# Optimization experiments

Hardware: AMD Instinct MI355X
Metric: run time of the kernel (lower is better)

Reference implementation:

```python
import jax, jax.numpy as jnp
import numpy as np

INPUT_SIZE = 32   # activity vocab
HIDDEN = 512
OUT = 33          # OUT-1 activity logits + 1 duration
COND = 128
LAYERS = 2
MAXLEN = 64
BATCH = 256
SOS = 0
SLOPE = 0.01      # LeakyReLU default negative slope

def _leaky(x):
    return jnp.where(x >= 0, x, SLOPE * x)

def setup_inputs() -> dict:
    key = jax.random.key(0)
    ks = jax.random.split(key, 16)
    s = 0.05  # small init scale keeps gates in a sane range
    return {
        "batch_size": BATCH,
        "h0": jax.random.normal(ks[0], (LAYERS, BATCH, HIDDEN), jnp.float32),
        "c0": jax.random.normal(ks[1], (LAYERS, BATCH, HIDDEN), jnp.float32),
        "conditionals": jax.random.normal(ks[2], (BATCH, COND), jnp.float32),
        "emb": jax.random.normal(ks[3], (INPUT_SIZE, HIDDEN - 1), jnp.float32) * s,
        "Wih": jax.random.normal(ks[4], (LAYERS, 4 * HIDDEN, HIDDEN), jnp.float32) * s,
        "Whh": jax.random.normal(ks[5], (LAYERS, 4 * HIDDEN, HIDDEN), jnp.float32) * s,
        "bih": jax.random.normal(ks[6], (LAYERS, 4 * HIDDEN), jnp.float32) * s,
        "bhh": jax.random.normal(ks[7], (LAYERS, 4 * HIDDEN), jnp.float32) * s,
        "fcW": jax.random.normal(ks[8], (HIDDEN, COND), jnp.float32) * s,
        "fcb": jax.random.normal(ks[9], (HIDDEN,), jnp.float32) * s,
        "fc2W": jax.random.normal(ks[10], (HIDDEN, HIDDEN), jnp.float32) * s,
        "fc2b": jax.random.normal(ks[11], (HIDDEN,), jnp.float32) * s,
        "fc3W": jax.random.normal(ks[12], (OUT, HIDDEN), jnp.float32) * s,
        "fc3b": jax.random.normal(ks[13], (OUT,), jnp.float32) * s,
    }

def reference(batch_size, h0, c0, conditionals, emb, Wih, Whh, bih, bhh,
              fcW, fcb, fc2W, fc2b, fc3W, fc3b):
    B = h0.shape[1]
    # conditionals branch is step-invariant: compute once (same math as per-step fc+LeakyReLU)
    cond = _leaky(conditionals @ fcW.T + fcb)  # [B, H]
    # decoder_input = zeros[B,1,2] with act channel = sos
    inp0 = jnp.concatenate(
        [jnp.full((B, 1), float(SOS), jnp.float32), jnp.zeros((B, 1), jnp.float32)], axis=-1)

    def step(carry, _):
        h, c, inp = carry  # h,c: [L,B,H], inp: [B,2]
        # CustomDurationEmbedding: embed act index, concat duration channel -> [B,H]
        x = jnp.concatenate([emb[inp[:, 0].astype(jnp.int32)], inp[:, 1:]], axis=-1)
        hs, cs = [], []
        for l in range(LAYERS):  # seq_len==1 per step -> one LSTM cell per layer
            g = x @ Wih[l].T + bih[l] + h[l] @ Whh[l].T + bhh[l]  # [B,4H]
            i_g, f_g, g_g, o_g = jnp.split(g, 4, axis=-1)         # torch gate order i,f,g,o
            c_l = jax.nn.sigmoid(f_g) * c[l] + jax.nn.sigmoid(i_g) * jnp.tanh(g_g)
            h_l = jax.nn.sigmoid(o_g) * jnp.tanh(c_l)
            hs.append(h_l); cs.append(c_l)
            x = h_l
        h_new, c_new = jnp.stack(hs), jnp.stack(cs)
        # conditional_add: (lstm_out + cond) -> fc2 -> LeakyReLU -> fc3
        pred = _leaky((x + cond) @ fc2W.T + fc2b) @ fc3W.T + fc3b  # [B,OUT]
        # pack: topk(1) over activity logits; softmax over singleton seq dim == 1.0
        act = jnp.argmax(pred[:, :OUT - 1], axis=-1).astype(pred.dtype)[:, None]
        dur = jnp.ones((B, 1), pred.dtype)
        nxt = jnp.concatenate([act, dur], axis=-1)
        return (h_new, c_new, nxt), pred

    _, outs = jax.lax.scan(step, (h0, c0, inp0), None, length=MAXLEN)  # [T,B,OUT]
    outs = jnp.transpose(outs, (1, 0, 2))  # [B,T,OUT]
    acts_log_probs = jax.nn.log_softmax(outs[..., :OUT - 1], axis=-1)
    durations = jax.nn.softmax(outs[..., OUT - 1:], axis=1)  # Softmax(dim=-2): over time
    return jnp.concatenate([acts_log_probs, durations], axis=-1)
```

## Files before the change

### kernel.cpp

```cpp
#include <hip/hip_runtime.h>
#include <math.h>

#define BB   256
#define HH   512
#define NWG  256
#define NTHR 1024
#define TT   64
#define NOUT 33
#define CD   128
#define SZ   (HH*BB)
#define LOFF (4*HH*HH)
#define BOFF (4*HH)
#define WBLK (16*1024)

typedef float f16v __attribute__((ext_vector_type(16)));
typedef float f8v  __attribute__((ext_vector_type(8)));
typedef const __attribute__((address_space(4))) float  cfloat;
typedef const __attribute__((address_space(4))) f16v   cf16v;
typedef const __attribute__((address_space(4))) f8v    cf8v;

__device__ __forceinline__ float sigm(float x)  { return 1.0f/(1.0f+expf(-x)); }
__device__ __forceinline__ float lrelu(float x) { return x >= 0.0f ? x : 0.01f*x; }

__device__ __forceinline__ float gld(const float* p) {
  return __hip_atomic_load(p, __ATOMIC_RELAXED, __HIP_MEMORY_SCOPE_AGENT);
}
__device__ __forceinline__ void gst(float* p, float v) {
  __hip_atomic_store(p, v, __ATOMIC_RELAXED, __HIP_MEMORY_SCOPE_AGENT);
}

__device__ __forceinline__ cfloat* cptr(const float* p) {
  unsigned long long u = (unsigned long long)p;
  unsigned lo = __builtin_amdgcn_readfirstlane((unsigned)u);
  unsigned hi = __builtin_amdgcn_readfirstlane((unsigned)(u >> 32));
  return (cfloat*)((((unsigned long long)hi) << 32) | (unsigned long long)lo);
}

__device__ __forceinline__ void gbar(unsigned* bar, unsigned ep, int grp, bool fence) {
  __syncthreads();
  if (threadIdx.x == 0) {
    if (fence) __builtin_amdgcn_fence(__ATOMIC_RELEASE, "agent");
    unsigned old = __hip_atomic_fetch_add(&bar[grp*16], 1u, __ATOMIC_RELAXED, __HIP_MEMORY_SCOPE_AGENT);
    if (old == ep*32u + 31u) {
      unsigned o2 = __hip_atomic_fetch_add(&bar[128], 1u, __ATOMIC_RELAXED, __HIP_MEMORY_SCOPE_AGENT);
      if (o2 == ep*8u + 7u)
        __hip_atomic_store(&bar[144], ep+1u, __ATOMIC_RELAXED, __HIP_MEMORY_SCOPE_AGENT);
    }
    while (__hip_atomic_load(&bar[144], __ATOMIC_RELAXED, __HIP_MEMORY_SCOPE_AGENT) < ep+1u)
      __builtin_amdgcn_s_sleep(1);
    if (fence) __builtin_amdgcn_fence(__ATOMIC_ACQUIRE, "agent");
  }
  __syncthreads();
}

extern "C" __global__ void __launch_bounds__(256)
transpose_weights(const float* __restrict__ Wih, const float* __restrict__ Whh,
                  float* __restrict__ wsT)
{
  const int w   = blockIdx.x;
  const int tid = threadIdx.x;
  float* dst = wsT + w*WBLK;
  #pragma unroll 1
  for (int j = 0; j < 64; ++j) {
    int i  = j*256 + tid;
    int ri = i >> 10, k = i & 1023;
    int l  = k >> 9,  kk = k & 511;
    int r2 = ri & 7,  u = r2 >> 2, g = r2 & 3;
    const float* src = (ri < 8) ? Wih : Whh;
    dst[k*16 + ri] = src[l*LOFF + (g*HH + 2*w + u)*HH + kk];
  }
}

__device__ __forceinline__ void FMA2(const f16v& w, float x0, float x1,
                                     float h0, float h1, float* acc) {
  #pragma unroll
  for (int r = 0; r < 8; ++r) {
    acc[r*2+0] += w[r]*x0;
    acc[r*2+1] += w[r]*x1;
  }
  #pragma unroll
  for (int r = 0; r < 8; ++r) {
    acc[r*2+0] += w[8+r]*h0;
    acc[r*2+1] += w[8+r]*h1;
  }
}

__device__ __forceinline__ void lstm_phase(const float* __restrict__ wT,
    const float* __restrict__ bias, float* __restrict__ red,
    const float* __restrict__ xsrc, const float* __restrict__ hsrc,
    float* __restrict__ hdst, float* __restrict__ cbuf,
    int hu0, int tid, int ks, int bg)
{
  const int lane  = tid & 63;
  const int kbase = ks*64;
  const int b0    = bg*128 + lane;
  cf16v* wk = (cf16v*)cptr(wT + kbase*16);
  const float* xp = xsrc + kbase*BB + b0;
  const float* hp = hsrc + kbase*BB + b0;

  float acc[16];
  #pragma unroll
  for (int r = 0; r < 16; ++r) acc[r] = 0.0f;

  float qx[4], qh[4], px[4], ph[4];
  #pragma unroll
  for (int j = 0; j < 2; ++j) {
    qx[j*2] = gld(xp + j*BB); qx[j*2+1] = gld(xp + j*BB + 64);
    qh[j*2] = gld(hp + j*BB); qh[j*2+1] = gld(hp + j*BB + 64);
  }
  #pragma unroll 1
  for (int it = 0; it < 32; ++it) {
    f16v w0 = wk[it*2+0];
    f16v w1 = wk[it*2+1];
    if (it+1 < 32) {
      #pragma unroll
      for (int j = 0; j < 2; ++j) {
        px[j*2]   = gld(xp + (it*2+2+j)*BB);  px[j*2+1] = gld(xp + (it*2+2+j)*BB + 64);
        ph[j*2]   = gld(hp + (it*2+2+j)*BB);  ph[j*2+1] = gld(hp + (it*2+2+j)*BB + 64);
      }
    }
    FMA2(w0, qx[0], qx[1], qh[0], qh[1], acc);
    FMA2(w1, qx[2], qx[3], qh[2], qh[3], acc);
    #pragma unroll
    for (int j = 0; j < 4; ++j) { qx[j] = px[j]; qh[j] = ph[j]; }
  }
  #pragma unroll
  for (int r = 0; r < 8; ++r) {
    red[(ks*8 + r)*BB + b0]      = acc[r*2];
    red[(ks*8 + r)*BB + b0 + 64] = acc[r*2+1];
  }
  __syncthreads();
  if (tid < 512) {
    const int b = tid & 255, u = tid >> 8;
    float g[4];
    #pragma unroll
    for (int gg = 0; gg < 4; ++gg) {
      float s = bias[u*4+gg];
      #pragma unroll
      for (int k2 = 0; k2 < 8; ++k2) s += red[(k2*8 + u*4+gg)*BB + b];
      g[gg] = s;
    }
    const int hu = hu0 + u;
    float ig = sigm(g[0]), fg = sigm(g[1]);
    float gv = tanhf(g[2]), og = sigm(g[3]);
    float cn = fg*cbuf[hu*BB+b] + ig*gv;
    cbuf[hu*BB+b] = cn;
    gst(hdst + hu*BB + b, og*tanhf(cn));
  }
}

extern "C" __global__ void __launch_bounds__(NTHR)
decoder_kernel(const float* __restrict__ h0, const float* __restrict__ c0,
               const float* __restrict__ conds, const float* __restrict__ emb,
               const float* __restrict__ wsT, const float* __restrict__ bih,
               const float* __restrict__ bhh, const float* __restrict__ fcW,
               const float* __restrict__ fcb, const float* __restrict__ fc2W,
               const float* __restrict__ fc2b, const float* __restrict__ fc3W,
               const float* __restrict__ fc3b,
               float* __restrict__ out, unsigned* bar, float* wsf)
{
  const int w   = blockIdx.x;
  const int tid = threadIdx.x;
  const int hu0 = 2*w;
  const int grp = w & 7;
  const int wv  = tid >> 6;
  const int bg  = wv & 1;
  const int ks  = wv >> 1;

  float* xbuf  = wsf;
  float* h1b0  = wsf + 1*SZ;
  float* h1b1  = wsf + 2*SZ;
  float* h2b0  = wsf + 3*SZ;
  float* h2b1  = wsf + 4*SZ;
  float* c1b   = wsf + 5*SZ;
  float* c2b   = wsf + 6*SZ;
  float* condb = wsf + 7*SZ;
  float* yb    = wsf + 8*SZ;
  float* condY = wsf + 9*SZ;

  const float* wT1 = wsT + w*WBLK;
  const float* wT2 = wsT + w*WBLK + 512*16;

  __shared__ float red[64*BB];
  __shared__ float bias1[8], bias2[8], biasc[2];
  __shared__ float lds_y[HH];
  __shared__ float part[NOUT][17];
  __shared__ int   lds_act;
  __shared__ float lds_pad[4096];
  if (tid == 0) ((volatile float*)lds_pad)[0] = 0.0f;

  if (tid < 512) {
    const int b = tid & 255, u = tid >> 8;
    const int k = hu0 + u;
    xbuf[k*BB+b] = (k < HH-1) ? emb[k] : 0.0f;
    h1b0[k*BB+b] = h0[b*HH + k];
    c1b [k*BB+b] = c0[b*HH + k];
    h2b0[k*BB+b] = h0[(BB+b)*HH + k];
    c2b [k*BB+b] = c0[(BB+b)*HH + k];
    float a = fcb[k];
    const float4* cp = (const float4*)(conds + b*CD);
    const float4* wp = (const float4*)(fcW + k*CD);
    #pragma unroll 8
    for (int q = 0; q < CD/4; ++q) {
      float4 c4 = cp[q], w4 = wp[q];
      a += c4.x*w4.x + c4.y*w4.y + c4.z*w4.z + c4.w*w4.w;
    }
    condb[k*BB+b] = lrelu(a);
  }
  if (tid < 8) {
    int u = tid >> 2, g = tid & 3;
    bias1[tid] = bih[g*HH + hu0 + u] + bhh[g*HH + hu0 + u];
    bias2[tid] = bih[BOFF + g*HH + hu0 + u] + bhh[BOFF + g*HH + hu0 + u];
  }
  if (tid < 2) biasc[tid] = fc2b[hu0 + tid];

  unsigned ep = 0;
  gbar(bar, ep++, grp, true);

  if (tid < 512) {
    const int b = tid & 255, u = tid >> 8;
    cfloat* wr = cptr(fc2W + (hu0+u)*HH);
    float s = 0.0f;
    #pragma unroll 4
    for (int k = 0; k < HH; k += 4) {
      s += wr[k]*condb[k*BB+b]     + wr[k+1]*condb[(k+1)*BB+b]
         + wr[k+2]*condb[(k+2)*BB+b] + wr[k+3]*condb[(k+3)*BB+b];
    }
    condY[(hu0+u)*BB + b] = s;
  }
  __syncthreads();

  for (int t = 0; t < TT; ++t) {
    const bool par = (t & 1) != 0;
    float* h1r = par ? h1b1 : h1b0;
    float* h1w = par ? h1b0 : h1b1;
    float* h2r = par ? h2b1 : h2b0;
    float* h2w = par ? h2b0 : h2b1;

    lstm_phase(wT1, bias1, red, xbuf, h1r, h1w, c1b, hu0, tid, ks, bg);
    gbar(bar, ep++, grp, false);
    lstm_phase(wT2, bias2, red, h1w, h2r, h2w, c2b, hu0, tid, ks, bg);
    gbar(bar, ep++, grp, false);
    {
      const int b = tid & 255, s4 = tid >> 8;
      const float* hp = h2w + (s4*128)*BB + b;
      cf8v* w0v = (cf8v*)cptr(fc2W + (hu0+0)*HH + s4*128);
      cf8v* w1v = (cf8v*)cptr(fc2W + (hu0+1)*HH + s4*128);
      float a0 = 0.0f, a1 = 0.0f;
      float q[8], pq[8];
      #pragma unroll
      for (int j = 0; j < 8; ++j) q[j] = gld(hp + j*BB);
      #pragma unroll 1
      for (int it = 0; it < 16; ++it) {
        f8v wa = w0v[it];
        f8v wb = w1v[it];
        if (it+1 < 16) {
          #pragma unroll
          for (int j = 0; j < 8; ++j) pq[j] = gld(hp + (it*8+8+j)*BB);
        }
        #pragma unroll
        for (int j = 0; j < 8; ++j) { a0 += wa[j]*q[j]; a1 += wb[j]*q[j]; }
        #pragma unroll
        for (int j = 0; j < 8; ++j) q[j] = pq[j];
      }
      red[(s4*2+0)*BB + b] = a0;
      red[(s4*2+1)*BB + b] = a1;
    }
    __syncthreads();
    if (tid < 512) {
      const int b = tid & 255, u = tid >> 8;
      float s = biasc[u] + condY[(hu0+u)*BB + b];
      #pragma unroll
      for (int s4 = 0; s4 < 4; ++s4) s += red[(s4*2+u)*BB + b];
      gst(yb + (hu0+u)*BB + b, lrelu(s));
    }
    gbar(bar, ep++, grp, false);
    {
      if (tid < 512) lds_y[tid] = gld(yb + tid*BB + w);
      __syncthreads();
      int o = 0, kc = 0;
      bool active = false;
      if (tid < 512)        { o = tid & 31; kc = tid >> 5; active = true; }
      else if (tid < 528)   { o = 32;       kc = tid - 512; active = true; }
      if (active) {
        float p = 0.0f;
        const float* fw = fc3W + o*HH + kc*32;
        #pragma unroll
        for (int k2 = 0; k2 < 32; ++k2) p += fw[k2] * lds_y[kc*32 + k2];
        part[o][kc] = p;
      }
      __syncthreads();
      float predv = -1e30f;
      if (tid < NOUT) {
        float s = fc3b[tid];
        #pragma unroll
        for (int kc2 = 0; kc2 < 16; ++kc2) s += part[tid][kc2];
        predv = s;
        out[(w*TT + t)*NOUT + tid] = s;
      }
      if (tid < 64) {
        float v  = (tid < 32) ? predv : -1e30f;
        int  idx = tid;
        #pragma unroll
        for (int off = 32; off > 0; off >>= 1) {
          float ov = __shfl_xor(v, off);
          int   oi = __shfl_xor(idx, off);
          if (ov > v || (ov == v && oi < idx)) { v = ov; idx = oi; }
        }
        if (tid == 0) lds_act = idx;
      }
      __syncthreads();
      const int act = lds_act;
      if (tid < 512)
        gst(xbuf + tid*BB + w, (tid < 511) ? emb[act*(HH-1) + tid] : 1.0f);
    }
    gbar(bar, ep++, grp, false);
  }

  if (tid < TT) {
    const int s = tid;
    float* po = out + (w*TT + s)*NOUT;
    float v[NOUT];
    #pragma unroll
    for (int o = 0; o < NOUT; ++o) v[o] = po[o];
    float m = v[0];
    #pragma unroll
    for (int o = 1; o < 32; ++o) m = fmaxf(m, v[o]);
    float sum = 0.0f;
    #pragma unroll
    for (int o = 0; o < 32; ++o) sum += expf(v[o] - m);
    float lse = m + logf(sum);
    #pragma unroll
    for (int o = 0; o < 32; ++o) po[o] = v[o] - lse;
    float d = v[32];
    float dm = d;
    #pragma unroll
    for (int off = 32; off > 0; off >>= 1) dm = fmaxf(dm, __shfl_xor(dm, off));
    float e = expf(d - dm);
    float es = e;
    #pragma unroll
    for (int off = 32; off > 0; off >>= 1) es += __shfl_xor(es, off);
    po[32] = e / es;
  }
}

extern "C" void kernel_launch(void* const* d_in, const int* in_sizes, int n_in,
                              void* d_out, int out_size, void* d_ws, size_t ws_size,
                              hipStream_t stream) {
  const float* h0   = (const float*)d_in[1];
  const float* c0   = (const float*)d_in[2];
  const float* cnd  = (const float*)d_in[3];
  const float* emb  = (const float*)d_in[4];
  const float* Wih  = (const float*)d_in[5];
  const float* Whh  = (const float*)d_in[6];
  const float* bih  = (const float*)d_in[7];
  const float* bhh  = (const float*)d_in[8];
  const float* fcW  = (const float*)d_in[9];
  const float* fcb  = (const float*)d_in[10];
  const float* fc2W = (const float*)d_in[11];
  const float* fc2b = (const float*)d_in[12];
  const float* fc3W = (const float*)d_in[13];
  const float* fc3b = (const float*)d_in[14];

  unsigned* bar = (unsigned*)d_ws;
  float* wsf = (float*)((char*)d_ws + 1024);
  float* wsT = wsf + 10*SZ;

  (void)hipMemsetAsync(d_ws, 0, 1024, stream);

  hipLaunchKernelGGL(transpose_weights, dim3(NWG), dim3(256), 0, stream,
                     Wih, Whh, wsT);
  hipLaunchKernelGGL(decoder_kernel, dim3(NWG), dim3(NTHR), 0, stream,
                     h0, c0, cnd, emb, wsT, bih, bhh, fcW, fcb,
                     fc2W, fc2b, fc3W, fc3b, (float*)d_out, bar, wsf);
}
```

Before: 3.731 ms.

## Retile LSTM decoder into 64 hidden-slices by 4 batch-groups with per-group barriers

Repartitions the persistent decoder so each of 256 workgroups owns 8 hidden units across a 64-batch tile instead of 2 hidden units across all 256 batches. Activations move to a k-interleaved float4 layout and are staged through double-buffered LDS while pre-transposed weights are read as scalar-uniform vectors. The grid barrier now synchronizes only the 64 workgroups sharing a batch group, and the cell state lives in registers. fc2 weights are also pre-transposed. This cuts grid-wide sync cost and global traffic per step, but it adds more LDS staging and syncthreads per phase.

```diff
diff --git a/kernel.cpp b/kernel.cpp
--- a/kernel.cpp
+++ b/kernel.cpp
@@ -3,21 +3,20 @@
 
 #define BB   256
 #define HH   512
-#define NWG  256
-#define NTHR 1024
 #define TT   64
 #define NOUT 33
 #define CD   128
-#define SZ   (HH*BB)
+#define NTHR 1024
 #define LOFF (4*HH*HH)
-#define BOFF (4*HH)
-#define WBLK (16*1024)
+
+#define HUT  8
+#define BT   64
+#define ABUF 131072
+#define FC2OFF 4194304
 
 typedef float f16v __attribute__((ext_vector_type(16)));
-typedef float f8v  __attribute__((ext_vector_type(8)));
-typedef const __attribute__((address_space(4))) float  cfloat;
-typedef const __attribute__((address_space(4))) f16v   cf16v;
-typedef const __attribute__((address_space(4))) f8v    cf8v;
+typedef const __attribute__((address_space(4))) float cfloat;
+typedef const __attribute__((address_space(4))) f16v  cf16v;
 
 __device__ __forceinline__ float sigm(float x)  { return 1.0f/(1.0f+expf(-x)); }
 __device__ __forceinline__ float lrelu(float x) { return x >= 0.0f ? x : 0.01f*x; }
@@ -27,6 +26,9 @@
 }
 __device__ __forceinline__ void gst(float* p, float v) {
   __hip_atomic_store(p, v, __ATOMIC_RELAXED, __HIP_MEMORY_SCOPE_AGENT);
+}
+__device__ __forceinline__ unsigned gldu(const unsigned* p) {
+  return __hip_atomic_load(p, __ATOMIC_RELAXED, __HIP_MEMORY_SCOPE_AGENT);
 }
 
 __device__ __forceinline__ cfloat* cptr(const float* p) {
@@ -36,247 +38,271 @@
   return (cfloat*)((((unsigned long long)hi) << 32) | (unsigned long long)lo);
 }
 
-__device__ __forceinline__ void gbar(unsigned* bar, unsigned ep, int grp, bool fence) {
+__device__ __forceinline__ void gbar(unsigned* bar, unsigned ep, int j) {
   __syncthreads();
   if (threadIdx.x == 0) {
-    if (fence) __builtin_amdgcn_fence(__ATOMIC_RELEASE, "agent");
-    unsigned old = __hip_atomic_fetch_add(&bar[grp*16], 1u, __ATOMIC_RELAXED, __HIP_MEMORY_SCOPE_AGENT);
-    if (old == ep*32u + 31u) {
-      unsigned o2 = __hip_atomic_fetch_add(&bar[128], 1u, __ATOMIC_RELAXED, __HIP_MEMORY_SCOPE_AGENT);
-      if (o2 == ep*8u + 7u)
-        __hip_atomic_store(&bar[144], ep+1u, __ATOMIC_RELAXED, __HIP_MEMORY_SCOPE_AGENT);
-    }
-    while (__hip_atomic_load(&bar[144], __ATOMIC_RELAXED, __HIP_MEMORY_SCOPE_AGENT) < ep+1u)
-      __builtin_amdgcn_s_sleep(1);
-    if (fence) __builtin_amdgcn_fence(__ATOMIC_ACQUIRE, "agent");
+    unsigned old = __hip_atomic_fetch_add(&bar[j*32], 1u, __ATOMIC_RELAXED, __HIP_MEMORY_SCOPE_AGENT);
+    if (old == ep*64u + 63u)
+      __hip_atomic_store(&bar[j*32+16], ep+1u, __ATOMIC_RELAXED, __HIP_MEMORY_SCOPE_AGENT);
+    while (gldu(&bar[j*32+16]) < ep+1u) __builtin_amdgcn_s_sleep(1);
   }
   __syncthreads();
 }
 
 extern "C" __global__ void __launch_bounds__(256)
 transpose_weights(const float* __restrict__ Wih, const float* __restrict__ Whh,
-                  float* __restrict__ wsT)
+                  const float* __restrict__ fc2W, float* __restrict__ wsT)
 {
-  const int w   = blockIdx.x;
-  const int tid = threadIdx.x;
-  float* dst = wsT + w*WBLK;
+  const int i = blockIdx.x, tid = threadIdx.x;
   #pragma unroll 1
-  for (int j = 0; j < 64; ++j) {
-    int i  = j*256 + tid;
-    int ri = i >> 10, k = i & 1023;
-    int l  = k >> 9,  kk = k & 511;
-    int r2 = ri & 7,  u = r2 >> 2, g = r2 & 3;
-    const float* src = (ri < 8) ? Wih : Whh;
-    dst[k*16 + ri] = src[l*LOFF + (g*HH + 2*w + u)*HH + kk];
-  }
-}
-
-__device__ __forceinline__ void FMA2(const f16v& w, float x0, float x1,
-                                     float h0, float h1, float* acc) {
-  #pragma unroll
-  for (int r = 0; r < 8; ++r) {
-    acc[r*2+0] += w[r]*x0;
-    acc[r*2+1] += w[r]*x1;
-  }
-  #pragma unroll
-  for (int r = 0; r < 8; ++r) {
-    acc[r*2+0] += w[8+r]*h0;
-    acc[r*2+1] += w[8+r]*h1;
-  }
-}
-
-__device__ __forceinline__ void lstm_phase(const float* __restrict__ wT,
-    const float* __restrict__ bias, float* __restrict__ red,
-    const float* __restrict__ xsrc, const float* __restrict__ hsrc,
-    float* __restrict__ hdst, float* __restrict__ cbuf,
-    int hu0, int tid, int ks, int bg)
+  for (int idx = tid; idx < 65536; idx += 256) {
+    int kj = idx & 3, r8 = (idx>>2)&7, kc = (idx>>5)&127, o = (idx>>12)&3, a = (idx>>14)&1, l = idx>>15;
+    int hu = i*HUT + 2*o + (r8>>2), g = r8&3, k = kc*4+kj;
+    const float* src = a ? Whh : Wih;
+    wsT[(size_t)i*65536 + idx] = src[(size_t)l*LOFF + (size_t)(g*HH + hu)*HH + k];
+  }
+  #pragma unroll 1
+  for (int idx = tid; idx < 4096; idx += 256) {
+    int kj = idx & 3, r8 = (idx>>2)&7, kc = idx>>5;
+    wsT[(size_t)FC2OFF + i*4096 + idx] = fc2W[(size_t)(i*HUT + r8)*HH + kc*4+kj];
+  }
+}
+
+__device__ __forceinline__ void stage_load(const float* src, int kcBase, int wv, int bglob, float4* st) {
+  #pragma unroll
+  for (int q = 0; q < 4; ++q) {
+    const float* p = src + (size_t)((kcBase + wv*4 + q)*256 + bglob)*4;
+    st[q].x = gld(p); st[q].y = gld(p+1); st[q].z = gld(p+2); st[q].w = gld(p+3);
+  }
+  __builtin_amdgcn_sched_barrier(0);
+}
+__device__ __forceinline__ void stage_write(float* buf, int wv, int lane, const float4* st) {
+  #pragma unroll
+  for (int q = 0; q < 4; ++q)
+    *(float4*)(buf + (wv*4+q)*256 + lane*4) = st[q];
+}
+
+template<int CNT>
+__device__ __forceinline__ void consume(const float* buf, cfloat* wb, int cstart, int lane, float* acc) {
+  #pragma unroll 1
+  for (int m = 0; m < CNT; ++m) {
+    int cL = cstart + m;
+    float4 q = *(const float4*)(buf + cL*256 + lane*4);
+    cf16v* wp = (cf16v*)(wb + (size_t)cL*32);
+    f16v wA = wp[0], wB = wp[1];
+    #pragma unroll
+    for (int r = 0; r < 4; ++r) {
+      acc[r]   += wA[r*4+0]*q.x + wA[r*4+1]*q.y + wA[r*4+2]*q.z + wA[r*4+3]*q.w;
+      acc[4+r] += wB[r*4+0]*q.x + wB[r*4+1]*q.y + wB[r*4+2]*q.z + wB[r*4+3]*q.w;
+    }
+  }
+}
+
+__device__ __forceinline__ void layer_phase(const float* xsrc, const float* hsrc,
+    const float* wsTL, float* hdst, float& creg, const float* ldsb,
+    float* T, int tid, int Bbase, int hugBase)
 {
-  const int lane  = tid & 63;
-  const int kbase = ks*64;
-  const int b0    = bg*128 + lane;
-  cf16v* wk = (cf16v*)cptr(wT + kbase*16);
-  const float* xp = xsrc + kbase*BB + b0;
-  const float* hp = hsrc + kbase*BB + b0;
-
-  float acc[16];
-  #pragma unroll
-  for (int r = 0; r < 16; ++r) acc[r] = 0.0f;
-
-  float qx[4], qh[4], px[4], ph[4];
-  #pragma unroll
-  for (int j = 0; j < 2; ++j) {
-    qx[j*2] = gld(xp + j*BB); qx[j*2+1] = gld(xp + j*BB + 64);
-    qh[j*2] = gld(hp + j*BB); qh[j*2+1] = gld(hp + j*BB + 64);
-  }
-  #pragma unroll 1
-  for (int it = 0; it < 32; ++it) {
-    f16v w0 = wk[it*2+0];
-    f16v w1 = wk[it*2+1];
-    if (it+1 < 32) {
+  const int lane = tid & 63, wv = tid >> 6;
+  const int o = wv & 3, sub = wv >> 2;
+  float* buf0 = T;
+  float* buf1 = T + 16384;
+  float acc[8];
+  #pragma unroll
+  for (int r = 0; r < 8; ++r) acc[r] = 0.f;
+  cfloat* wx0 = cptr(wsTL + o*4096);
+  cfloat* wx1 = cptr(wsTL + o*4096 + 2048);
+  cfloat* wh0 = cptr(wsTL + 16384 + o*4096);
+  cfloat* wh1 = cptr(wsTL + 16384 + o*4096 + 2048);
+
+  float4 st[4];
+  stage_load(xsrc, 0, wv, Bbase + lane, st);
+  stage_write(buf0, wv, lane, st);
+  __syncthreads();
+  stage_load(xsrc, 64, wv, Bbase + lane, st);
+  consume<16>(buf0, wx0, sub*16, lane, acc);
+  stage_write(buf1, wv, lane, st);
+  __syncthreads();
+  stage_load(hsrc, 0, wv, Bbase + lane, st);
+  consume<16>(buf1, wx1, sub*16, lane, acc);
+  stage_write(buf0, wv, lane, st);
+  __syncthreads();
+  stage_load(hsrc, 64, wv, Bbase + lane, st);
+  consume<16>(buf0, wh0, sub*16, lane, acc);
+  stage_write(buf1, wv, lane, st);
+  __syncthreads();
+  consume<16>(buf1, wh1, sub*16, lane, acc);
+  __syncthreads();
+  #pragma unroll
+  for (int r = 0; r < 8; ++r) T[(sub*32 + o*8 + r)*64 + lane] = acc[r];
+  __syncthreads();
+  if (tid < 512) {
+    int hu = tid >> 6, b = tid & 63;
+    float g[4];
+    #pragma unroll
+    for (int gg = 0; gg < 4; ++gg) {
+      int gr = hu*4 + gg;
+      float s = ldsb[gr];
       #pragma unroll
-      for (int j = 0; j < 2; ++j) {
-        px[j*2]   = gld(xp + (it*2+2+j)*BB);  px[j*2+1] = gld(xp + (it*2+2+j)*BB + 64);
-        ph[j*2]   = gld(hp + (it*2+2+j)*BB);  ph[j*2+1] = gld(hp + (it*2+2+j)*BB + 64);
-      }
-    }
-    FMA2(w0, qx[0], qx[1], qh[0], qh[1], acc);
-    FMA2(w1, qx[2], qx[3], qh[2], qh[3], acc);
-    #pragma unroll
-    for (int j = 0; j < 4; ++j) { qx[j] = px[j]; qh[j] = ph[j]; }
-  }
-  #pragma unroll
-  for (int r = 0; r < 8; ++r) {
-    red[(ks*8 + r)*BB + b0]      = acc[r*2];
-    red[(ks*8 + r)*BB + b0 + 64] = acc[r*2+1];
-  }
-  __syncthreads();
-  if (tid < 512) {
-    const int b = tid & 255, u = tid >> 8;
-    float g[4];
-    #pragma unroll
-    for (int gg = 0; gg < 4; ++gg) {
-      float s = bias[u*4+gg];
-      #pragma unroll
-      for (int k2 = 0; k2 < 8; ++k2) s += red[(k2*8 + u*4+gg)*BB + b];
+      for (int sb = 0; sb < 4; ++sb) s += T[(sb*32 + gr)*64 + b];
       g[gg] = s;
     }
-    const int hu = hu0 + u;
-    float ig = sigm(g[0]), fg = sigm(g[1]);
-    float gv = tanhf(g[2]), og = sigm(g[3]);
-    float cn = fg*cbuf[hu*BB+b] + ig*gv;
-    cbuf[hu*BB+b] = cn;
-    gst(hdst + hu*BB + b, og*tanhf(cn));
-  }
+    float ig = sigm(g[0]), fg = sigm(g[1]), gv = tanhf(g[2]), og = sigm(g[3]);
+    float cn = fg*creg + ig*gv;
+    creg = cn;
+    int hug = hugBase + hu, bg = Bbase + b;
+    gst(hdst + (size_t)((hug>>2)*256 + bg)*4 + (hug&3), og*tanhf(cn));
+  }
+  __syncthreads();
+}
+
+__device__ __forceinline__ void fc2_phase(const float* h2src, const float* wsTf,
+    float* ybuf, const float* lds_bc, float condY, float* T, int tid, int Bbase, int hugBase)
+{
+  const int lane = tid & 63, wv = tid >> 6;
+  float* buf0 = T;
+  float* buf1 = T + 16384;
+  float acc[8];
+  #pragma unroll
+  for (int r = 0; r < 8; ++r) acc[r] = 0.f;
+  cfloat* w0 = cptr(wsTf);
+  cfloat* w1 = cptr(wsTf + 2048);
+
+  float4 st[4];
+  stage_load(h2src, 0, wv, Bbase + lane, st);
+  stage_write(buf0, wv, lane, st);
+  __syncthreads();
+  stage_load(h2src, 64, wv, Bbase + lane, st);
+  consume<4>(buf0, w0, wv*4, lane, acc);
+  stage_write(buf1, wv, lane, st);
+  __syncthreads();
+  consume<4>(buf1, w1, wv*4, lane, acc);
+  __syncthreads();
+  #pragma unroll
+  for (int r = 0; r < 8; ++r) T[(wv*8 + r)*64 + lane] = acc[r];
+  __syncthreads();
+  if (tid < 512) {
+    int row = tid >> 6, b = tid & 63;
+    float s = lds_bc[row] + condY;
+    #pragma unroll
+    for (int w16 = 0; w16 < 16; ++w16) s += T[(w16*8 + row)*64 + b];
+    int rg = hugBase + row, bg = Bbase + b;
+    gst(ybuf + (size_t)((rg>>2)*256 + bg)*4 + (rg&3), lrelu(s));
+  }
+  __syncthreads();
 }
 
 extern "C" __global__ void __launch_bounds__(NTHR)
 decoder_kernel(const float* __restrict__ h0, const float* __restrict__ c0,
                const float* __restrict__ conds, const float* __restrict__ emb,
-               const float* __restrict__ wsT, const float* __restrict__ bih,
-               const float* __restrict__ bhh, const float* __restrict__ fcW,
-               const float* __restrict__ fcb, const float* __restrict__ fc2W,
+               const float* __restrict__ bih, const float* __restrict__ bhh,
+               const float* __restrict__ fcW, const float* __restrict__ fcb,
                const float* __restrict__ fc2b, const float* __restrict__ fc3W,
                const float* __restrict__ fc3b,
                float* __restrict__ out, unsigned* bar, float* wsf)
 {
-  const int w   = blockIdx.x;
+  const int w = blockIdx.x;
+  const int i = w & 63, j = w >> 6;
   const int tid = threadIdx.x;
-  const int hu0 = 2*w;
-  const int grp = w & 7;
-  const int wv  = tid >> 6;
-  const int bg  = wv & 1;
-  const int ks  = wv >> 1;
-
-  float* xbuf  = wsf;
-  float* h1b0  = wsf + 1*SZ;
-  float* h1b1  = wsf + 2*SZ;
-  float* h2b0  = wsf + 3*SZ;
-  float* h2b1  = wsf + 4*SZ;
-  float* c1b   = wsf + 5*SZ;
-  float* c2b   = wsf + 6*SZ;
-  float* condb = wsf + 7*SZ;
-  float* yb    = wsf + 8*SZ;
-  float* condY = wsf + 9*SZ;
-
-  const float* wT1 = wsT + w*WBLK;
-  const float* wT2 = wsT + w*WBLK + 512*16;
-
-  __shared__ float red[64*BB];
-  __shared__ float bias1[8], bias2[8], biasc[2];
+  const int lane = tid & 63, wv = tid >> 6;
+  const int Bbase = j*BT;
+  const int hugBase = i*HUT;
+
+  float* xbuf = wsf;
+  float* h1a = wsf + 1*ABUF;
+  float* h1b = wsf + 2*ABUF;
+  float* h2a = wsf + 3*ABUF;
+  float* h2b = wsf + 4*ABUF;
+  float* ybuf = wsf + 5*ABUF;
+  const float* wsT  = wsf + 6*ABUF;
+  const float* wsTf = wsT + FC2OFF + i*4096;
+
+  __shared__ float4 T4[8192];
+  float* T = (float*)T4;
   __shared__ float lds_y[HH];
   __shared__ float part[NOUT][17];
+  __shared__ float lds_b1[32], lds_b2[32], lds_bc[8];
   __shared__ int   lds_act;
-  __shared__ float lds_pad[4096];
-  if (tid == 0) ((volatile float*)lds_pad)[0] = 0.0f;
-
+
+  if (tid < 32) {
+    int hu = hugBase + (tid>>2), g = tid&3;
+    lds_b1[tid] = bih[g*HH+hu] + bhh[g*HH+hu];
+    lds_b2[tid] = bih[4*HH + g*HH+hu] + bhh[4*HH + g*HH+hu];
+  }
+  if (tid < 8) lds_bc[tid] = fc2b[hugBase + tid];
+
+  float c1 = 0.f, c2 = 0.f;
   if (tid < 512) {
-    const int b = tid & 255, u = tid >> 8;
-    const int k = hu0 + u;
-    xbuf[k*BB+b] = (k < HH-1) ? emb[k] : 0.0f;
-    h1b0[k*BB+b] = h0[b*HH + k];
-    c1b [k*BB+b] = c0[b*HH + k];
-    h2b0[k*BB+b] = h0[(BB+b)*HH + k];
-    c2b [k*BB+b] = c0[(BB+b)*HH + k];
-    float a = fcb[k];
-    const float4* cp = (const float4*)(conds + b*CD);
-    const float4* wp = (const float4*)(fcW + k*CD);
-    #pragma unroll 8
-    for (int q = 0; q < CD/4; ++q) {
-      float4 c4 = cp[q], w4 = wp[q];
-      a += c4.x*w4.x + c4.y*w4.y + c4.z*w4.z + c4.w*w4.w;
+    int hu = tid>>6, b = tid&63;
+    int hug = hugBase + hu, bg = Bbase + b;
+    c1 = c0[(size_t)bg*HH + hug];
+    c2 = c0[(size_t)(BB+bg)*HH + hug];
+    gst(h1a + (size_t)((hug>>2)*256 + bg)*4 + (hug&3), h0[(size_t)bg*HH+hug]);
+    gst(h2a + (size_t)((hug>>2)*256 + bg)*4 + (hug&3), h0[(size_t)(BB+bg)*HH+hug]);
+  }
+  #pragma unroll 1
+  for (int it = 0; it < 32; ++it) {
+    int idx = tid + it*1024;
+    int kj = idx&3, b = (idx>>2)&63, kc = idx>>8;
+    int k = kc*4+kj;
+    gst(xbuf + (size_t)(kc*256 + Bbase+b)*4 + kj, (k < HH-1) ? emb[k] : 0.0f);
+  }
+
+  {
+    int b = tid&63, kcg = tid>>6;
+    const float* crow = conds + (size_t)(Bbase+b)*CD;
+    #pragma unroll 1
+    for (int it = 0; it < 8; ++it) {
+      int kc = kcg + it*16;
+      float4 v;
+      #pragma unroll
+      for (int kj = 0; kj < 4; ++kj) {
+        int k = kc*4+kj;
+        const float* fr = fcW + (size_t)k*CD;
+        float s = fcb[k];
+        #pragma unroll 4
+        for (int q = 0; q < CD; q += 4)
+          s += fr[q]*crow[q] + fr[q+1]*crow[q+1] + fr[q+2]*crow[q+2] + fr[q+3]*crow[q+3];
+        ((float*)&v)[kj] = lrelu(s);
+      }
+      *(float4*)(T + kc*256 + b*4) = v;
     }
-    condb[k*BB+b] = lrelu(a);
-  }
-  if (tid < 8) {
-    int u = tid >> 2, g = tid & 3;
-    bias1[tid] = bih[g*HH + hu0 + u] + bhh[g*HH + hu0 + u];
-    bias2[tid] = bih[BOFF + g*HH + hu0 + u] + bhh[BOFF + g*HH + hu0 + u];
-  }
-  if (tid < 2) biasc[tid] = fc2b[hu0 + tid];
-
-  unsigned ep = 0;
-  gbar(bar, ep++, grp, true);
-
-  if (tid < 512) {
-    const int b = tid & 255, u = tid >> 8;
-    cfloat* wr = cptr(fc2W + (hu0+u)*HH);
-    float s = 0.0f;
-    #pragma unroll 4
-    for (int k = 0; k < HH; k += 4) {
-      s += wr[k]*condb[k*BB+b]     + wr[k+1]*condb[(k+1)*BB+b]
-         + wr[k+2]*condb[(k+2)*BB+b] + wr[k+3]*condb[(k+3)*BB+b];
-    }
-    condY[(hu0+u)*BB + b] = s;
-  }
-  __syncthreads();
-
-  for (int t = 0; t < TT; ++t) {
-    const bool par = (t & 1) != 0;
-    float* h1r = par ? h1b1 : h1b0;
-    float* h1w = par ? h1b0 : h1b1;
-    float* h2r = par ? h2b1 : h2b0;
-    float* h2w = par ? h2b0 : h2b1;
-
-    lstm_phase(wT1, bias1, red, xbuf, h1r, h1w, c1b, hu0, tid, ks, bg);
-    gbar(bar, ep++, grp, false);
-    lstm_phase(wT2, bias2, red, h1w, h2r, h2w, c2b, hu0, tid, ks, bg);
-    gbar(bar, ep++, grp, false);
-    {
-      const int b = tid & 255, s4 = tid >> 8;
-      const float* hp = h2w + (s4*128)*BB + b;
-      cf8v* w0v = (cf8v*)cptr(fc2W + (hu0+0)*HH + s4*128);
-      cf8v* w1v = (cf8v*)cptr(fc2W + (hu0+1)*HH + s4*128);
-      float a0 = 0.0f, a1 = 0.0f;
-      float q[8], pq[8];
-      #pragma unroll
-      for (int j = 0; j < 8; ++j) q[j] = gld(hp + j*BB);
-      #pragma unroll 1
-      for (int it = 0; it < 16; ++it) {
-        f8v wa = w0v[it];
-        f8v wb = w1v[it];
-        if (it+1 < 16) {
-          #pragma unroll
-          for (int j = 0; j < 8; ++j) pq[j] = gld(hp + (it*8+8+j)*BB);
-        }
-        #pragma unroll
-        for (int j = 0; j < 8; ++j) { a0 += wa[j]*q[j]; a1 += wb[j]*q[j]; }
-        #pragma unroll
-        for (int j = 0; j < 8; ++j) q[j] = pq[j];
-      }
-      red[(s4*2+0)*BB + b] = a0;
-      red[(s4*2+1)*BB + b] = a1;
-    }
+  }
+  __syncthreads();
+  float condY = 0.f;
+  {
+    float accy[8];
+    #pragma unroll
+    for (int r = 0; r < 8; ++r) accy[r] = 0.f;
+    consume<8>(T, cptr(wsTf), wv*8, lane, accy);
+    __syncthreads();
+    #pragma unroll
+    for (int r = 0; r < 8; ++r) T[(wv*8+r)*64 + lane] = accy[r];
     __syncthreads();
     if (tid < 512) {
-      const int b = tid & 255, u = tid >> 8;
-      float s = biasc[u] + condY[(hu0+u)*BB + b];
+      int row = tid>>6, b = tid&63;
       #pragma unroll
-      for (int s4 = 0; s4 < 4; ++s4) s += red[(s4*2+u)*BB + b];
-      gst(yb + (hu0+u)*BB + b, lrelu(s));
+      for (int w16 = 0; w16 < 16; ++w16) condY += T[(w16*8+row)*64 + b];
     }
-    gbar(bar, ep++, grp, false);
+  }
+
+  unsigned ep = 0;
+  gbar(bar, ep++, j);
+
+  for (int t = 0; t < TT; ++t) {
+    float* h1r = (t&1)? h1b : h1a;
+    float* h1w = (t&1)? h1a : h1b;
+    float* h2r = (t&1)? h2b : h2a;
+    float* h2w = (t&1)? h2a : h2b;
+
+    layer_phase(xbuf, h1r, wsT + (size_t)(i*2+0)*32768, h1w, c1, lds_b1, T, tid, Bbase, hugBase);
+    gbar(bar, ep++, j);
+    layer_phase(h1w, h2r, wsT + (size_t)(i*2+1)*32768, h2w, c2, lds_b2, T, tid, Bbase, hugBase);
+    gbar(bar, ep++, j);
+    fc2_phase(h2w, wsTf, ybuf, lds_bc, condY, T, tid, Bbase, hugBase);
+    gbar(bar, ep++, j);
     {
-      if (tid < 512) lds_y[tid] = gld(yb + tid*BB + w);
+      if (tid < 512)
+        lds_y[tid] = gld(ybuf + (size_t)((tid>>2)*256 + w)*4 + (tid&3));
       __syncthreads();
       int o = 0, kc = 0;
       bool active = false;
@@ -284,7 +310,7 @@
       else if (tid < 528)   { o = 32;       kc = tid - 512; active = true; }
       if (active) {
         float p = 0.0f;
-        const float* fw = fc3W + o*HH + kc*32;
+        const float* fw = fc3W + (size_t)o*HH + kc*32;
         #pragma unroll
         for (int k2 = 0; k2 < 32; ++k2) p += fw[k2] * lds_y[kc*32 + k2];
         part[o][kc] = p;
@@ -296,7 +322,7 @@
         #pragma unroll
         for (int kc2 = 0; kc2 < 16; ++kc2) s += part[tid][kc2];
         predv = s;
-        out[(w*TT + t)*NOUT + tid] = s;
+        out[(size_t)(w*TT + t)*NOUT + tid] = s;
       }
       if (tid < 64) {
         float v  = (tid < 32) ? predv : -1e30f;
@@ -312,14 +338,15 @@
       __syncthreads();
       const int act = lds_act;
       if (tid < 512)
-        gst(xbuf + tid*BB + w, (tid < 511) ? emb[act*(HH-1) + tid] : 1.0f);
+        gst(xbuf + (size_t)((tid>>2)*256 + w)*4 + (tid&3),
+            (tid < HH-1) ? emb[(size_t)act*(HH-1) + tid] : 1.0f);
     }
-    gbar(bar, ep++, grp, false);
+    gbar(bar, ep++, j);
   }
 
   if (tid < TT) {
     const int s = tid;
-    float* po = out + (w*TT + s)*NOUT;
+    float* po = out + (size_t)(w*TT + s)*NOUT;
     float v[NOUT];
     #pragma unroll
     for (int o = 0; o < NOUT; ++o) v[o] = po[o];
@@ -364,13 +391,13 @@
 
   unsigned* bar = (unsigned*)d_ws;
   float* wsf = (float*)((char*)d_ws + 1024);
-  float* wsT = wsf + 10*SZ;
+  float* wsT = wsf + 6*ABUF;
 
   (void)hipMemsetAsync(d_ws, 0, 1024, stream);
 
-  hipLaunchKernelGGL(transpose_weights, dim3(NWG), dim3(256), 0, stream,
-                     Wih, Whh, wsT);
-  hipLaunchKernelGGL(decoder_kernel, dim3(NWG), dim3(NTHR), 0, stream,
-                     h0, c0, cnd, emb, wsT, bih, bhh, fcW, fcb,
-                     fc2W, fc2b, fc3W, fc3b, (float*)d_out, bar, wsf);
-}
+  hipLaunchKernelGGL(transpose_weights, dim3(64), dim3(256), 0, stream,
+                     Wih, Whh, fc2W, wsT);
+  hipLaunchKernelGGL(decoder_kernel, dim3(256), dim3(NTHR), 0, stream,
+                     h0, c0, cnd, emb, bih, bhh, fcW, fcb,
+                     fc2b, fc3W, fc3b, (float*)d_out, bar, wsf);
+}
```

After: 12.96 ms. 247% more time.
